# Kernel tuning notes

Measured on AMD Instinct MI355X. Metric: run time of the kernel, lower is better.

The kernel has to match this reference:

```python
import jax, jax.numpy as jnp
import numpy as np
from jax import lax

RNN_H = 384      # rnnHiddenSize
HID = 384        # hiddenSize (LSTMCell input size)
POS_EMB = 128    # posEmbSize
POS_NUM = 32
LABELS = 33
BATCH = 16
CHAR_NUM = 1024
ENC = 2 * RNN_H  # 768


def setup_inputs() -> dict:
    key = jax.random.key(0)
    ks = jax.random.split(key, 12)

    def xav(k, shape):
        fan_in = shape[-1]
        return jax.random.normal(k, shape, jnp.float32) / np.sqrt(fan_in)

    return {
        "encoder_output": jax.random.normal(ks[0], (BATCH, CHAR_NUM, ENC), jnp.float32),
        "char_sizes": jax.random.randint(ks[1], (BATCH,), 1, CHAR_NUM, jnp.int32),
        "label_is_sep": jax.random.randint(ks[2], (LABELS,), 0, 2, jnp.int32),
        "label_pos_id": jax.random.randint(ks[3], (LABELS,), 0, POS_NUM, jnp.int32),
        "posEmb": xav(ks[4], (POS_NUM, POS_EMB)),
        "W_ih": xav(ks[5], (4 * RNN_H, HID)),
        "W_hh": xav(ks[6], (4 * RNN_H, RNN_H)),
        "b_ih": jnp.zeros((4 * RNN_H,), jnp.float32),
        "b_hh": jnp.zeros((4 * RNN_H,), jnp.float32),
        "W_lin": xav(ks[7], (LABELS, RNN_H + ENC)),
        "b_lin": jnp.zeros((LABELS,), jnp.float32),
        "W_cmb": xav(ks[8], (HID, ENC + POS_EMB)),
        "b_cmb": jnp.zeros((HID,), jnp.float32),
    }


def reference(encoder_output, char_sizes, label_is_sep, label_pos_id, posEmb,
              W_ih, W_hh, b_ih, b_hh, W_lin, b_lin, W_cmb, b_cmb):
    def lstm_cell(x, h, c):
        g = x @ W_ih.T + b_ih + h @ W_hh.T + b_hh
        i, f, gg, o = jnp.split(g, 4)
        c2 = jax.nn.sigmoid(f) * c + jax.nn.sigmoid(i) * jnp.tanh(gg)
        h2 = jax.nn.sigmoid(o) * jnp.tanh(c2)
        return h2, c2

    def decode(enc, size):  # enc: [T, 2H]; size: scalar int
        T = enc.shape[0]
        # prefix sums make the variable-length avg_pool1d a two-gather op
        prefix = jnp.concatenate([jnp.zeros((1, ENC), enc.dtype),
                                  jnp.cumsum(enc, axis=0)], axis=0)  # [T+1, 2H]

        # initial LSTM step on the (zero) initial last_word_pos_emb
        h, c = lstm_cell(jnp.zeros((HID,), enc.dtype),
                         jnp.zeros((RNN_H,), enc.dtype),
                         jnp.zeros((RNN_H,), enc.dtype))
        zero = jnp.int32(0)
        carry = (h, c, jnp.zeros((POS_EMB,), enc.dtype), zero, zero, zero, zero)

        def step(carry, inp):
            t, enc_t = inp
            h, c, lpe, wlen, nw, npos, plast = carry
            valid = t < size
            out = jnp.tanh(jnp.concatenate([h, enc_t]) @ W_lin.T + b_lin)  # [L]
            aid = jnp.argmax(out)
            is_sep = label_is_sep[aid] > 0
            sep = is_sep & valid
            app = (~is_sep) & valid

            wl_prev = wlen  # length of word that becomes words[-2] on a SEP
            npos_new = jnp.where(sep, npos + 1, npos)
            nw_new = jnp.where(sep, nw + 1, jnp.where(app, jnp.maximum(nw, 1), nw))
            # state.last_pos = pos_id[-2] (the pos before this one), then embed
            lpe_new = jnp.where(sep & (npos_new >= 2), posEmb[plast], lpe)
            plast_new = jnp.where(sep, label_pos_id[aid], plast)
            wlen_new = jnp.where(sep, jnp.int32(1),
                                 jnp.where(app, wlen + 1, wlen))

            # avg_pool1d over previous word chars enc[t-wl_prev : t]
            denom = jnp.maximum(wl_prev, 1).astype(enc.dtype)
            start = jnp.maximum(t - wl_prev, 0)
            avg = (prefix[t] - prefix[start]) / denom  # [2H]
            lwp = jnp.tanh(jnp.concatenate([lpe_new, avg]) @ W_cmb.T + b_cmb)
            h2, c2 = lstm_cell(lwp, h, c)
            do_lstm = sep & (nw_new >= 2)
            h_new = jnp.where(do_lstm, h2, h)
            c_new = jnp.where(do_lstm, c2, c)

            out = jnp.where(valid, out, jnp.zeros_like(out))  # bucket rows
            return (h_new, c_new, lpe_new, wlen_new, nw_new, npos_new, plast_new), out

        _, outs = lax.scan(step, carry, (jnp.arange(T, dtype=jnp.int32), enc))
        return outs  # [T, L]

    outs = jax.vmap(decode)(encoder_output, char_sizes)  # [B, T, L]
    B, T, L = outs.shape
    return jax.nn.log_softmax(outs.reshape(B * T, L), axis=-1)
```

## Files before the change

kernel.cpp:

```cpp
#include <hip/hip_runtime.h>
#include <math.h>


namespace {
constexpr int NB = 16;
constexpr int NT = 1024;
constexpr int NE = 768;
constexpr int NH = 384;
constexpr int NL = 33;
constexpr int ROUNDS = 1024;
constexpr int NSLICE = 16;
constexpr int JS = 24;
constexpr int RS = 96;

constexpr size_t OFF_SL   = 0;
constexpr size_t N_SL     = (size_t)NSLICE * NE * RS;
constexpr size_t OFF_PEW  = OFF_SL + N_SL;
constexpr size_t N_PEW    = 32 * NH;
constexpr size_t OFF_ENCW = OFF_PEW + N_PEW;
constexpr size_t N_ENCW   = (size_t)NB * NT * NL;
constexpr size_t OFF_BS   = OFF_ENCW + N_ENCW;
constexpr size_t OFF_PC   = OFF_BS + 2048;
constexpr size_t N_PC     = (size_t)NB * 1025 * NH;
constexpr size_t OFF_STATE = OFF_PC + N_PC;
constexpr size_t ST_STRIDE = 4096;
constexpr int SX_HWBP = 64;
constexpr int SX_H    = 1280;
constexpr int SX_C    = 2432;
constexpr int IX_T = 0, IX_WLEN = 1, IX_NW = 2, IX_NPOS = 3, IX_PLAST = 4,
              IX_LPEP = 5, IX_LPEE = 6, IX_DONE = 7;
}

__device__ __forceinline__ float sigmf(float x) { return 1.0f / (1.0f + expf(-x)); }

__global__ void k_prep(const float* __restrict__ W_ih, const float* __restrict__ W_hh,
                       const float* __restrict__ W_cmb, const float* __restrict__ posEmb,
                       float* __restrict__ ws) {
    float* SL = ws + OFF_SL;
    float* pw = ws + OFF_PEW;
    const int n1 = (int)N_SL, n2 = (int)N_PEW;
    for (int i = blockIdx.x * blockDim.x + threadIdx.x; i < n1 + n2;
         i += gridDim.x * blockDim.x) {
        if (i < n1) {
            int sl = i / (NE * RS), rem = i % (NE * RS);
            int k = rem / RS, rho = rem % RS;
            int gate = rho / JS, jj = rho % JS;
            int grow = gate * NH + sl * JS + jj;
            SL[i] = (k < NH) ? W_ih[(size_t)grow * NH + k]
                             : W_hh[(size_t)grow * NH + (k - NH)];
        } else {
            int j3 = i - n1;
            int p = j3 / NH, j = j3 % NH;
            const float* pe = posEmb + p * 128;
            const float* wr = W_cmb + (size_t)j * 896;
            float a = 0.f;
            #pragma unroll 4
            for (int k = 0; k < 128; ++k) a += pe[k] * wr[k];
            pw[j3] = a;
        }
    }
}

__global__ void k_encw(const float* __restrict__ enc, const float* __restrict__ W_lin,
                       float* __restrict__ ws) {
    float* encW = ws + OFF_ENCW;
    int gid = blockIdx.x * 256 + threadIdx.x;
    if (gid >= NB * NT * NL) return;
    int bt = gid / NL, l = gid % NL;
    const float4* e4 = (const float4*)(enc + (size_t)bt * NE);
    const float4* w4 = (const float4*)(W_lin + (size_t)l * 1152 + NH);
    float a0 = 0, a1 = 0, a2 = 0, a3 = 0;
    for (int k = 0; k < NE / 4; ++k) {
        float4 e = e4[k], w = w4[k];
        a0 += e.x * w.x; a1 += e.y * w.y; a2 += e.z * w.z; a3 += e.w * w.w;
    }
    encW[gid] = (a0 + a1) + (a2 + a3);
}

__global__ void k_encCmb(const float* __restrict__ enc, const float* __restrict__ W_cmb,
                         float* __restrict__ ws) {
    __shared__ float tile[16][NE];
    float* pc = ws + OFF_PC;
    int blk = blockIdx.x;
    int b = blk >> 6;
    int t0 = (blk & 63) * 16;
    for (int i = threadIdx.x; i < 16 * NE; i += 384) {
        int row = i / NE, k = i % NE;
        tile[row][k] = enc[((size_t)(b * NT + t0 + row)) * NE + k];
    }
    __syncthreads();
    int j = threadIdx.x;
    const float4* w4 = (const float4*)(W_cmb + (size_t)j * 896 + 128);
    float acc[16];
    #pragma unroll
    for (int r = 0; r < 16; ++r) acc[r] = 0.f;
    for (int q = 0; q < NE / 4; ++q) {
        float4 w = w4[q];
        #pragma unroll
        for (int r = 0; r < 16; ++r) {
            acc[r] += w.x * tile[r][q * 4] + w.y * tile[r][q * 4 + 1]
                    + w.z * tile[r][q * 4 + 2] + w.w * tile[r][q * 4 + 3];
        }
    }
    #pragma unroll
    for (int r = 0; r < 16; ++r)
        pc[((size_t)b * 1025 + t0 + r) * NH + j] = acc[r];
}

__global__ void k_prefix(float* __restrict__ ws) {
    float* pc = ws + OFF_PC;
    int id = blockIdx.x * 256 + threadIdx.x;
    if (id >= NB * NH) return;
    int b = id / NH, j = id % NH;
    float* p = pc + ((size_t)b * 1025) * NH + j;
    float s = 0.f;
    for (int t = 0; t < NT; ++t) {
        float x = p[(size_t)t * NH];
        p[(size_t)t * NH] = s;
        s += x;
    }
    p[(size_t)NT * NH] = s;
}

__global__ void k_init(const float* __restrict__ b_ih, const float* __restrict__ b_hh,
                       const float* __restrict__ W_lin, const float* __restrict__ b_lin,
                       float* __restrict__ ws) {
    __shared__ float shh[NH], shc[NH], shw[NL];
    int tid = threadIdx.x;
    if (tid < NH) {
        float gi = b_ih[tid] + b_hh[tid];
        float gg = b_ih[2 * NH + tid] + b_hh[2 * NH + tid];
        float go = b_ih[3 * NH + tid] + b_hh[3 * NH + tid];
        float c = sigmf(gi) * tanhf(gg);
        float h = sigmf(go) * tanhf(c);
        shh[tid] = h; shc[tid] = c;
    }
    __syncthreads();
    if (tid < NL) {
        float a = b_lin[tid];
        for (int k = 0; k < NH; ++k) a += W_lin[(size_t)tid * 1152 + k] * shh[k];
        shw[tid] = a;
    }
    for (int i = tid; i < 4 * NH; i += 1024) ws[OFF_BS + i] = b_ih[i] + b_hh[i];
    __syncthreads();
    for (int s = 0; s < NB; ++s) {
        float* stf = ws + OFF_STATE + (size_t)s * ST_STRIDE;
        int* ii = (int*)stf;
        if (tid < 16) ii[tid] = (tid == IX_LPEP || tid == IX_LPEE) ? -1 : 0;
        if (tid >= 32 && tid < 32 + 576) {
            int i2 = tid - 32, r = i2 / 36, l = i2 % 36;
            stf[SX_HWBP + i2] = (r == 0 && l < NL) ? (shw[l] - b_lin[l]) : 0.f;
        }
        if (tid < NH) { stf[SX_H + tid] = shh[tid]; stf[SX_C + tid] = shc[tid]; }
    }
}

__global__ void k_fill(float* __restrict__ out) {
    int i = blockIdx.x * 256 + threadIdx.x;
    if (i < NB * NT * NL) out[i] = 0.f;
}

__global__ __launch_bounds__(384) void k_round(
    const int* __restrict__ char_sizes,
    const int* __restrict__ label_is_sep, const int* __restrict__ label_pos_id,
    const float* __restrict__ W_lin, const float* __restrict__ b_lin,
    const float* __restrict__ b_cmb, float* __restrict__ ws,
    float* __restrict__ out, const int slot) {

    const int bid = blockIdx.x;
    const int s = bid >> 4;
    const int rh = bid & 15;
    const int tid = threadIdx.x;
    const int lane = tid & 63;
    const int wave = tid >> 6;

    float* stf = ws + OFF_STATE + (size_t)s * ST_STRIDE;
    int* ir = (int*)stf + slot * 16;
    int* iw = (int*)stf + (slot ^ 1) * 16;
    if (ir[IX_DONE]) return;

    const float* hWbp_r = stf + SX_HWBP + slot * 576;
    float*       hWbp_w = stf + SX_HWBP + (slot ^ 1) * 576;
    const float* h_r    = stf + SX_H + slot * 512;
    float*       h_w    = stf + SX_H + (slot ^ 1) * 512;
    float*       cst    = stf + SX_C;

    const float* SLw  = ws + OFF_SL + (size_t)rh * (NE * RS);
    const float* pew  = ws + OFF_PEW;
    const float* encW = ws + OFF_ENCW;
    const float* bsum = ws + OFF_BS;
    const float* pcb  = ws + OFF_PC + (size_t)s * 1025 * NH;

    __shared__ float sh_hWb[40], sh_h[NH], sh_x[NH], sh_part[384], sh_ph[288];
    __shared__ float sh_g[RS], sh_h2[JS];
    __shared__ int sh_issep[NL], sh_posid[NL], sh_scan[8];

    sh_h[tid] = h_r[tid];
    float creg = (tid < JS) ? cst[rh * JS + tid] : 0.f;
    __syncthreads();

    if (wave == 0) {
        if (lane < NL) {
            sh_issep[lane] = label_is_sep[lane];
            sh_posid[lane] = label_pos_id[lane];
            float a = b_lin[lane];
            #pragma unroll
            for (int i = 0; i < 16; ++i) a += hWbp_r[i * 36 + lane];
            sh_hWb[lane] = a;
        }
        asm volatile("" ::: "memory");

        int t = ir[IX_T], wlen = ir[IX_WLEN], nw = ir[IX_NW], npos = ir[IX_NPOS],
            plast = ir[IX_PLAST], lpe_pend = ir[IX_LPEP], lpe_eff = ir[IX_LPEE];
        int size = char_sizes[s]; if (size > NT) size = NT;
        const float* eWb = encW + (size_t)s * NT * NL;
        float* outb = out + (size_t)s * NT * NL;
        int evt_t = -1, evt_start = 0; float evt_den = 1.f;

        for (; t < size; ++t) {
            float ot = (lane < NL) ? tanhf(eWb[(size_t)t * NL + lane] + sh_hWb[lane]) : -INFINITY;
            float bv = ot; int bi = lane;
            #pragma unroll
            for (int d = 32; d; d >>= 1) {
                float ov = __shfl_xor(bv, d);
                int   oi = __shfl_xor(bi, d);
                if (ov > bv || (ov == bv && oi < bi)) { bv = ov; bi = oi; }
            }
            const int aid = bi;
            if (rh == 0 && lane < NL) outb[(size_t)t * NL + lane] = ot;
            const int issep = sh_issep[aid];
            const int wl_prev = wlen;
            int nw_new;
            if (issep) { npos += 1; nw_new = nw + 1; }
            else       { nw_new = (nw < 1) ? 1 : nw; }
            const int do_l = issep && (nw_new >= 2);
            if (issep && npos >= 2) lpe_pend = plast;
            if (issep) plast = sh_posid[aid];
            wlen = issep ? 1 : wlen + 1;
            nw = nw_new;
            if (do_l) {
                evt_t = t;
                evt_start = (t - wl_prev < 0) ? 0 : (t - wl_prev);
                evt_den = (float)((wl_prev < 1) ? 1 : wl_prev);
                if (lpe_pend >= 0) { lpe_eff = lpe_pend; lpe_pend = -1; }
                ++t;
                break;
            }
        }

        if (lane == 0) {
            sh_scan[0] = evt_t; sh_scan[1] = evt_start;
            sh_scan[2] = __float_as_int(evt_den); sh_scan[3] = lpe_eff;
            if (rh == 0) {
                if (evt_t < 0) {
                    iw[IX_DONE] = 1; ir[IX_DONE] = 1;
                } else {
                    iw[IX_T] = t; iw[IX_WLEN] = wlen; iw[IX_NW] = nw;
                    iw[IX_NPOS] = npos; iw[IX_PLAST] = plast;
                    iw[IX_LPEP] = lpe_pend; iw[IX_LPEE] = lpe_eff;
                    iw[IX_DONE] = 0;
                }
            }
        }
    } else if (tid >= 64 && tid < 352) {
        const int u = tid - 64;
        const int ci = u / 96, rho = u - ci * 96;
        const float* wp = SLw + (size_t)(NH + ci * 128) * RS + rho;
        const float* xp = sh_h + ci * 128;
        float a0 = 0.f, a1 = 0.f, a2 = 0.f, a3 = 0.f;
        #pragma unroll 8
        for (int k = 0; k < 128; k += 4) {
            a0 += wp[(size_t)(k + 0) * RS] * xp[k + 0];
            a1 += wp[(size_t)(k + 1) * RS] * xp[k + 1];
            a2 += wp[(size_t)(k + 2) * RS] * xp[k + 2];
            a3 += wp[(size_t)(k + 3) * RS] * xp[k + 3];
        }
        sh_ph[ci * 96 + rho] = (a0 + a1) + (a2 + a3);
    }
    __syncthreads();

    const int evt_t = sh_scan[0];
    if (evt_t < 0) return;
    const int evt_start = sh_scan[1];
    const float evt_den = __int_as_float(sh_scan[2]);
    const int lpe_eff = sh_scan[3];

    {
        const int j = tid;
        float avg = (pcb[(size_t)evt_t * NH + j] - pcb[(size_t)evt_start * NH + j]) / evt_den;
        float pv = (lpe_eff >= 0) ? pew[lpe_eff * NH + j] : 0.f;
        sh_x[j] = tanhf(pv + avg + b_cmb[j]);
    }
    __syncthreads();

    {
        const int kq = tid / 96, rho = tid - kq * 96;
        const float* wp = SLw + (size_t)(kq * 96) * RS + rho;
        const float* xp = sh_x + kq * 96;
        float a0 = 0.f, a1 = 0.f, a2 = 0.f, a3 = 0.f;
        #pragma unroll 8
        for (int k = 0; k < 96; k += 4) {
            a0 += wp[(size_t)(k + 0) * RS] * xp[k + 0];
            a1 += wp[(size_t)(k + 1) * RS] * xp[k + 1];
            a2 += wp[(size_t)(k + 2) * RS] * xp[k + 2];
            a3 += wp[(size_t)(k + 3) * RS] * xp[k + 3];
        }
        sh_part[tid] = (a0 + a1) + (a2 + a3);
    }
    __syncthreads();

    if (tid < RS) {
        const int gate = tid / JS, jj = tid % JS;
        const int grow = gate * NH + rh * JS + jj;
        sh_g[tid] = (((sh_part[tid] + sh_part[96 + tid])
                    + (sh_part[192 + tid] + sh_part[288 + tid]))
                   + ((sh_ph[tid] + sh_ph[96 + tid]) + sh_ph[192 + tid]))
                  + bsum[grow];
    }
    __syncthreads();
    if (tid < JS) {
        float gi = sh_g[tid], gf = sh_g[JS + tid];
        float gg = sh_g[2 * JS + tid], go = sh_g[3 * JS + tid];
        float c2 = sigmf(gf) * creg + sigmf(gi) * tanhf(gg);
        float h2 = sigmf(go) * tanhf(c2);
        cst[rh * JS + tid] = c2;
        h_w[rh * JS + tid] = h2;
        sh_h2[tid] = h2;
    }
    __syncthreads();
    if (tid < NL) {
        const float* wr = W_lin + (size_t)tid * 1152 + rh * JS;
        float a = 0.f;
        #pragma unroll
        for (int k = 0; k < JS; ++k) a += wr[k] * sh_h2[k];
        hWbp_w[rh * 36 + tid] = a;
    }
}

__global__ void k_post(float* __restrict__ out) {
    int row = blockIdx.x * 4 + (threadIdx.x >> 6);
    int lane = threadIdx.x & 63;
    if (row >= NB * NT) return;
    float* p = out + (size_t)row * NL;
    float x = (lane < NL) ? p[lane] : -INFINITY;
    float m = x;
    #pragma unroll
    for (int d = 32; d; d >>= 1) m = fmaxf(m, __shfl_xor(m, d));
    float e = (lane < NL) ? expf(x - m) : 0.f;
    float su = e;
    #pragma unroll
    for (int d = 32; d; d >>= 1) su += __shfl_xor(su, d);
    if (lane < NL) p[lane] = (x - m) - logf(su);
}

extern "C" void kernel_launch(void* const* d_in, const int* in_sizes, int n_in,
                              void* d_out, int out_size, void* d_ws, size_t ws_size,
                              hipStream_t stream) {
    const float* enc          = (const float*)d_in[0];
    const int*   char_sizes   = (const int*)d_in[1];
    const int*   label_is_sep = (const int*)d_in[2];
    const int*   label_pos_id = (const int*)d_in[3];
    const float* posEmb       = (const float*)d_in[4];
    const float* W_ih         = (const float*)d_in[5];
    const float* W_hh         = (const float*)d_in[6];
    const float* b_ih         = (const float*)d_in[7];
    const float* b_hh         = (const float*)d_in[8];
    const float* W_lin        = (const float*)d_in[9];
    const float* b_lin        = (const float*)d_in[10];
    const float* W_cmb        = (const float*)d_in[11];
    const float* b_cmb        = (const float*)d_in[12];
    float* out = (float*)d_out;
    float* ws  = (float*)d_ws;

    hipLaunchKernelGGL(k_prep, dim3(1024), dim3(256), 0, stream,
                       W_ih, W_hh, W_cmb, posEmb, ws);
    hipLaunchKernelGGL(k_encw, dim3((NB * NT * NL + 255) / 256), dim3(256), 0, stream,
                       enc, W_lin, ws);
    hipLaunchKernelGGL(k_encCmb, dim3(1024), dim3(384), 0, stream, enc, W_cmb, ws);
    hipLaunchKernelGGL(k_prefix, dim3((NB * NH + 255) / 256), dim3(256), 0, stream, ws);
    hipLaunchKernelGGL(k_init, dim3(1), dim3(1024), 0, stream,
                       b_ih, b_hh, W_lin, b_lin, ws);
    hipLaunchKernelGGL(k_fill, dim3((NB * NT * NL + 255) / 256), dim3(256), 0, stream, out);

    for (int r = 0; r < ROUNDS; ++r) {
        hipLaunchKernelGGL(k_round, dim3(256), dim3(384), 0, stream,
                           char_sizes, label_is_sep, label_pos_id,
                           W_lin, b_lin, b_cmb, ws, out, r & 1);
    }

    hipLaunchKernelGGL(k_post, dim3((NB * NT + 3) / 4), dim3(256), 0, stream, out);
}
```

Baseline: 6.904 ms.

## Transpose LSTM weight slices for float4 loads and finish tail in single-block kernel

The LSTM weight slices are transposed to row-major per gate row so the matvec loops read contiguous float4 vectors instead of strided scalars. The number of multi-block round launches drops from 1024 to 640, and a new per-sequence single-block kernel runs whatever decode steps remain sequentially, with no further kernel launches or cross-block exchange. This is meant to cut per-round launch overhead for the long tail where few sequences are still active. The trade-off is that each finish block does the full 1536x768 matvec alone, and its loop is capped at 1100 iterations.

```diff
diff --git a/kernel.cpp b/kernel.cpp
--- a/kernel.cpp
+++ b/kernel.cpp
@@ -8,13 +8,13 @@
 constexpr int NE = 768;
 constexpr int NH = 384;
 constexpr int NL = 33;
-constexpr int ROUNDS = 1024;
+constexpr int ROUNDS = 640;
 constexpr int NSLICE = 16;
 constexpr int JS = 24;
 constexpr int RS = 96;
 
 constexpr size_t OFF_SL   = 0;
-constexpr size_t N_SL     = (size_t)NSLICE * NE * RS;
+constexpr size_t N_SL     = (size_t)NSLICE * RS * NE;
 constexpr size_t OFF_PEW  = OFF_SL + N_SL;
 constexpr size_t N_PEW    = 32 * NH;
 constexpr size_t OFF_ENCW = OFF_PEW + N_PEW;
@@ -42,8 +42,8 @@
     for (int i = blockIdx.x * blockDim.x + threadIdx.x; i < n1 + n2;
          i += gridDim.x * blockDim.x) {
         if (i < n1) {
-            int sl = i / (NE * RS), rem = i % (NE * RS);
-            int k = rem / RS, rho = rem % RS;
+            int sl = i / (RS * NE), rem = i % (RS * NE);
+            int rho = rem / NE, k = rem % NE;
             int gate = rho / JS, jj = rho % JS;
             int grow = gate * NH + sl * JS + jj;
             SL[i] = (k < NH) ? W_ih[(size_t)grow * NH + k]
@@ -185,13 +185,15 @@
     float*       h_w    = stf + SX_H + (slot ^ 1) * 512;
     float*       cst    = stf + SX_C;
 
-    const float* SLw  = ws + OFF_SL + (size_t)rh * (NE * RS);
+    const float* SLw  = ws + OFF_SL + (size_t)rh * (RS * NE);
     const float* pew  = ws + OFF_PEW;
     const float* encW = ws + OFF_ENCW;
     const float* bsum = ws + OFF_BS;
     const float* pcb  = ws + OFF_PC + (size_t)s * 1025 * NH;
 
-    __shared__ float sh_hWb[40], sh_h[NH], sh_x[NH], sh_part[384], sh_ph[288];
+    __shared__ __align__(16) float sh_h[NH];
+    __shared__ __align__(16) float sh_x[NH];
+    __shared__ float sh_hWb[40], sh_part[384], sh_ph[288];
     __shared__ float sh_g[RS], sh_h2[JS];
     __shared__ int sh_issep[NL], sh_posid[NL], sh_scan[8];
 
@@ -265,17 +267,16 @@
     } else if (tid >= 64 && tid < 352) {
         const int u = tid - 64;
         const int ci = u / 96, rho = u - ci * 96;
-        const float* wp = SLw + (size_t)(NH + ci * 128) * RS + rho;
-        const float* xp = sh_h + ci * 128;
-        float a0 = 0.f, a1 = 0.f, a2 = 0.f, a3 = 0.f;
-        #pragma unroll 8
-        for (int k = 0; k < 128; k += 4) {
-            a0 += wp[(size_t)(k + 0) * RS] * xp[k + 0];
-            a1 += wp[(size_t)(k + 1) * RS] * xp[k + 1];
-            a2 += wp[(size_t)(k + 2) * RS] * xp[k + 2];
-            a3 += wp[(size_t)(k + 3) * RS] * xp[k + 3];
-        }
-        sh_ph[ci * 96 + rho] = (a0 + a1) + (a2 + a3);
+        const float4* wp = (const float4*)(SLw + (size_t)rho * NE + NH + ci * 128);
+        const float4* xp = (const float4*)(sh_h + ci * 128);
+        float4 acc = {0.f, 0.f, 0.f, 0.f};
+        #pragma unroll
+        for (int q = 0; q < 32; ++q) {
+            float4 w = wp[q], x = xp[q];
+            acc.x += w.x * x.x; acc.y += w.y * x.y;
+            acc.z += w.z * x.z; acc.w += w.w * x.w;
+        }
+        sh_ph[ci * 96 + rho] = (acc.x + acc.y) + (acc.z + acc.w);
     }
     __syncthreads();
 
@@ -295,17 +296,16 @@
 
     {
         const int kq = tid / 96, rho = tid - kq * 96;
-        const float* wp = SLw + (size_t)(kq * 96) * RS + rho;
-        const float* xp = sh_x + kq * 96;
-        float a0 = 0.f, a1 = 0.f, a2 = 0.f, a3 = 0.f;
-        #pragma unroll 8
-        for (int k = 0; k < 96; k += 4) {
-            a0 += wp[(size_t)(k + 0) * RS] * xp[k + 0];
-            a1 += wp[(size_t)(k + 1) * RS] * xp[k + 1];
-            a2 += wp[(size_t)(k + 2) * RS] * xp[k + 2];
-            a3 += wp[(size_t)(k + 3) * RS] * xp[k + 3];
-        }
-        sh_part[tid] = (a0 + a1) + (a2 + a3);
+        const float4* wp = (const float4*)(SLw + (size_t)rho * NE + kq * 96);
+        const float4* xp = (const float4*)(sh_x + kq * 96);
+        float4 acc = {0.f, 0.f, 0.f, 0.f};
+        #pragma unroll
+        for (int q = 0; q < 24; ++q) {
+            float4 w = wp[q], x = xp[q];
+            acc.x += w.x * x.x; acc.y += w.y * x.y;
+            acc.z += w.z * x.z; acc.w += w.w * x.w;
+        }
+        sh_part[tid] = (acc.x + acc.y) + (acc.z + acc.w);
     }
     __syncthreads();
 
@@ -334,6 +334,142 @@
         #pragma unroll
         for (int k = 0; k < JS; ++k) a += wr[k] * sh_h2[k];
         hWbp_w[rh * 36 + tid] = a;
+    }
+}
+
+__global__ __launch_bounds__(384) void k_finish(
+    const int* __restrict__ char_sizes,
+    const int* __restrict__ label_is_sep, const int* __restrict__ label_pos_id,
+    const float* __restrict__ W_lin, const float* __restrict__ b_lin,
+    const float* __restrict__ b_cmb, float* __restrict__ ws,
+    float* __restrict__ out) {
+
+    const int s = blockIdx.x, tid = threadIdx.x;
+    const int lane = tid & 63, wave = tid >> 6;
+    float* stf = ws + OFF_STATE + (size_t)s * ST_STRIDE;
+    int* ii = (int*)stf;
+    if (ii[IX_DONE]) return;
+
+    const float* SLT  = ws + OFF_SL;
+    const float* pew  = ws + OFF_PEW;
+    const float* bsum = ws + OFF_BS;
+    const float* pcb  = ws + OFF_PC + (size_t)s * 1025 * NH;
+    const float* eWb  = ws + OFF_ENCW + (size_t)s * NT * NL;
+    float* outb = out + (size_t)s * NT * NL;
+
+    __shared__ __align__(16) float sh_h[NH];
+    __shared__ __align__(16) float sh_x[NH];
+    __shared__ float sh_red[264], sh_hWb[40];
+    __shared__ int sh_issep[NL], sh_posid[NL], sh_scan[8];
+
+    sh_h[tid] = stf[SX_H + tid];
+    float creg = stf[SX_C + tid];
+    if (tid < NL) { sh_issep[tid] = label_is_sep[tid]; sh_posid[tid] = label_pos_id[tid]; }
+    int t = ii[IX_T], wlen = ii[IX_WLEN], nw = ii[IX_NW], npos = ii[IX_NPOS],
+        plast = ii[IX_PLAST], lpe_pend = ii[IX_LPEP], lpe_eff = ii[IX_LPEE];
+    int size = char_sizes[s]; if (size > NT) size = NT;
+    __syncthreads();
+
+    for (int iter = 0; iter < 1100; ++iter) {
+        if (tid < 264) {
+            const int l = tid >> 3, p = tid & 7;
+            const float* wr = W_lin + (size_t)l * 1152 + p * 48;
+            const float* hp = sh_h + p * 48;
+            float a = 0.f;
+            #pragma unroll
+            for (int k = 0; k < 48; ++k) a += wr[k] * hp[k];
+            sh_red[tid] = a;
+        }
+        __syncthreads();
+        if (tid < NL) {
+            float q = b_lin[tid];
+            #pragma unroll
+            for (int p = 0; p < 8; ++p) q += sh_red[tid * 8 + p];
+            sh_hWb[tid] = q;
+        }
+        __syncthreads();
+
+        if (wave == 0) {
+            int evt_t = -1, evt_start = 0; float evt_den = 1.f;
+            for (; t < size; ++t) {
+                float ot = (lane < NL) ? tanhf(eWb[(size_t)t * NL + lane] + sh_hWb[lane]) : -INFINITY;
+                float bv = ot; int bi = lane;
+                #pragma unroll
+                for (int d = 32; d; d >>= 1) {
+                    float ov = __shfl_xor(bv, d);
+                    int   oi = __shfl_xor(bi, d);
+                    if (ov > bv || (ov == bv && oi < bi)) { bv = ov; bi = oi; }
+                }
+                const int aid = bi;
+                if (lane < NL) outb[(size_t)t * NL + lane] = ot;
+                const int issep = sh_issep[aid];
+                const int wl_prev = wlen;
+                int nw_new;
+                if (issep) { npos += 1; nw_new = nw + 1; }
+                else       { nw_new = (nw < 1) ? 1 : nw; }
+                const int do_l = issep && (nw_new >= 2);
+                if (issep && npos >= 2) lpe_pend = plast;
+                if (issep) plast = sh_posid[aid];
+                wlen = issep ? 1 : wlen + 1;
+                nw = nw_new;
+                if (do_l) {
+                    evt_t = t;
+                    evt_start = (t - wl_prev < 0) ? 0 : (t - wl_prev);
+                    evt_den = (float)((wl_prev < 1) ? 1 : wl_prev);
+                    if (lpe_pend >= 0) { lpe_eff = lpe_pend; lpe_pend = -1; }
+                    ++t;
+                    break;
+                }
+            }
+            if (lane == 0) {
+                sh_scan[0] = evt_t; sh_scan[1] = evt_start;
+                sh_scan[2] = __float_as_int(evt_den); sh_scan[3] = lpe_eff;
+            }
+        }
+        __syncthreads();
+        const int evt_t = sh_scan[0];
+        if (evt_t < 0) break;
+        const int evt_start = sh_scan[1];
+        const float evt_den = __int_as_float(sh_scan[2]);
+        const int lpe_e = sh_scan[3];
+
+        {
+            const int j = tid;
+            float avg = (pcb[(size_t)evt_t * NH + j] - pcb[(size_t)evt_start * NH + j]) / evt_den;
+            float pv = (lpe_e >= 0) ? pew[lpe_e * NH + j] : 0.f;
+            sh_x[j] = tanhf(pv + avg + b_cmb[j]);
+        }
+        __syncthreads();
+
+        const int sl = tid / JS, jj = tid - sl * JS;
+        const float* base = SLT + (size_t)sl * (RS * NE);
+        float gv[4];
+        #pragma unroll
+        for (int g4 = 0; g4 < 4; ++g4) {
+            const float4* wp = (const float4*)(base + (size_t)(g4 * JS + jj) * NE);
+            const float4* xp = (const float4*)sh_x;
+            const float4* hp = (const float4*)sh_h;
+            float4 acc = {0.f, 0.f, 0.f, 0.f};
+            #pragma unroll 8
+            for (int q = 0; q < 96; ++q) {
+                float4 w = wp[q], x = xp[q];
+                acc.x += w.x * x.x; acc.y += w.y * x.y;
+                acc.z += w.z * x.z; acc.w += w.w * x.w;
+            }
+            #pragma unroll 8
+            for (int q = 0; q < 96; ++q) {
+                float4 w = wp[96 + q], h = hp[q];
+                acc.x += w.x * h.x; acc.y += w.y * h.y;
+                acc.z += w.z * h.z; acc.w += w.w * h.w;
+            }
+            gv[g4] = (acc.x + acc.y) + (acc.z + acc.w) + bsum[g4 * NH + tid];
+        }
+        float c2 = sigmf(gv[1]) * creg + sigmf(gv[0]) * tanhf(gv[2]);
+        float h2 = sigmf(gv[3]) * tanhf(c2);
+        creg = c2;
+        __syncthreads();
+        sh_h[tid] = h2;
+        __syncthreads();
     }
 }
 
@@ -387,6 +523,9 @@
                            char_sizes, label_is_sep, label_pos_id,
                            W_lin, b_lin, b_cmb, ws, out, r & 1);
     }
+    hipLaunchKernelGGL(k_finish, dim3(NB), dim3(384), 0, stream,
+                       char_sizes, label_is_sep, label_pos_id,
+                       W_lin, b_lin, b_cmb, ws, out);
 
     hipLaunchKernelGGL(k_post, dim3((NB * NT + 3) / 4), dim3(256), 0, stream, out);
 }
```

New measurement: 8.786 ms. 1.27x slower.
